# Kernel optimization log

Measured on AMD Instinct MI355X. Metric: run time of the kernel, lower is better.

Reference implementation:

```python
import jax, jax.numpy as jnp
import numpy as np

KHS = 3        # kernel_half_size
SIGMA = 1.6    # sigma / dx
DX = 1.0
C = 20.0       # accumulate() hard-codes c = 20


def _gauss_kernel():
    size = 2 * KHS + 1
    g = np.arange(size, dtype=np.float32) - (size - 1) / 2.0
    g = np.exp(-(g / SIGMA) ** 2 / 2.0) / (SIGMA * np.sqrt(2.0 * np.pi))
    k = g[:, None, None] * g[None, :, None] * g[None, None, :]
    k = k / k.sum()
    return jnp.asarray(k[None, None], dtype=jnp.float32)  # [1,1,7,7,7]


def _smooth(x, kernel):
    # depthwise (single-channel) 3d gaussian conv, 'same' padding, zero bias
    return jax.lax.conv_general_dilated(
        x, kernel, window_strides=(1, 1, 1),
        padding=[(KHS, KHS)] * 3,
        dimension_numbers=("NCDHW", "OIDHW", "NCDHW"))


def _fdiff(f, axis):
    # forward difference, replicate last difference to keep size (torchJacobian3 style)
    d = jnp.diff(f, axis=axis)
    last = jax.lax.slice_in_dim(d, d.shape[axis] - 1, d.shape[axis], axis=axis)
    return jnp.concatenate([d, last], axis=axis)


def _curl(v):
    # v: [B,3,D,H,W]; per-channel fields are [B,D,H,W]; z->axis1, y->axis2, x->axis3
    u, vv, w = v[:, 0], v[:, 1], v[:, 2]
    cu = _fdiff(w, 2) - _fdiff(vv, 1)   # dw/dy - dv/dz
    cv = _fdiff(u, 1) - _fdiff(w, 3)    # du/dz - dw/dx
    cw = _fdiff(vv, 3) - _fdiff(u, 2)   # dv/dx - du/dy
    return jnp.stack([cu, cv, cw], axis=1)


def _integrate(t, v):
    # trapezoidal transmittance-weighted integral along depth (dim 2)
    front = (1.0 - t[:, :, 0]) * v[:, :, 0]
    trap = jnp.sum((t[:, :, :-1] - t[:, :, 1:]) * (v[:, :, :-1] + v[:, :, 1:]) * 0.5, axis=2)
    return front + trap


def setup_inputs() -> dict:
    key = jax.random.key(0)
    k1, k2 = jax.random.split(key)
    d = jax.random.uniform(k1, (4, 1, 128, 128, 128), dtype=jnp.float32)
    v = jax.random.normal(k2, (4, 3, 128, 128, 128), dtype=jnp.float32)
    return {"d": d, "v": v}


def reference(d, v):
    kern = _gauss_kernel()
    ds = _smooth(d, kern)
    vort = _curl(v) / DX
    vn = jnp.sqrt(jnp.sum(vort ** 2, axis=1, keepdims=True))  # [B,1,D,H,W]
    vn = _smooth(vn, kern)
    # single default view dir 'zp' -> identity rotation
    df = jnp.flip(ds, axis=2)
    vf = jnp.flip(vn, axis=2)
    x = jnp.cumsum(df * DX, axis=2)
    t = (x * C + 1.0) * jnp.exp(-C * x)
    iv = _integrate(t, vf)              # [B,1,H,W]
    return jnp.clip(iv, 0.0, 1.0)
```

## Files before the change

kernel.cpp:

```cpp
#include <hip/hip_runtime.h>
#include <math.h>

#define NB 4
#define DD 128
#define HH 128
#define WW 128
#define VOX (DD*HH*WW)
#define NVOX (NB*VOX)

struct GaussW { float w[7]; };
struct CurlIn { float4 wc, wyn, vc, vzn, uc, uzn, uyn; float wxp, vxp; };

__device__ __forceinline__ float4 f4zero() { float4 z; z.x = z.y = z.z = z.w = 0.f; return z; }

__device__ __forceinline__ CurlIn curl4_load(const float* __restrict__ u,
                                             const float* __restrict__ vv,
                                             const float* __restrict__ w,
                                             int z, int y, int x0) {
    int xq = x0 >> 2;
    size_t s = ((size_t)z << 14) | ((size_t)y << 7) | (size_t)x0;
    int dy = (y < 127) ? 128 : -128;
    int dz = (z < 127) ? 16384 : -16384;
    int dxp = (xq < 31) ? 4 : 0;
    CurlIn ci;
    ci.wc  = *(const float4*)(w  + s);
    ci.wyn = *(const float4*)(w  + s + dy);
    ci.vc  = *(const float4*)(vv + s);
    ci.vzn = *(const float4*)(vv + s + dz);
    ci.uc  = *(const float4*)(u  + s);
    ci.uzn = *(const float4*)(u  + s + dz);
    ci.uyn = *(const float4*)(u  + s + dy);
    ci.wxp = w [s + 3 + dxp];
    ci.vxp = vv[s + 3 + dxp];
    return ci;
}

__device__ __forceinline__ float4 curl4_math(const CurlIn& ci, int z, int y, int x0) {
    float sy = (y < 127) ? 1.f : -1.f;
    float sz = (z < 127) ? 1.f : -1.f;
    float wca[4] = {ci.wc.x, ci.wc.y, ci.wc.z, ci.wc.w};
    float vca[4] = {ci.vc.x, ci.vc.y, ci.vc.z, ci.vc.w};
    float wya[4] = {ci.wyn.x, ci.wyn.y, ci.wyn.z, ci.wyn.w};
    float vza[4] = {ci.vzn.x, ci.vzn.y, ci.vzn.z, ci.vzn.w};
    float uca[4] = {ci.uc.x, ci.uc.y, ci.uc.z, ci.uc.w};
    float uza[4] = {ci.uzn.x, ci.uzn.y, ci.uzn.z, ci.uzn.w};
    float uya[4] = {ci.uyn.x, ci.uyn.y, ci.uyn.z, ci.uyn.w};
    float wsh[4] = {ci.wc.y, ci.wc.z, ci.wc.w, ci.wxp};
    float vsh[4] = {ci.vc.y, ci.vc.z, ci.vc.w, ci.vxp};

    float4 o;
    float* oa = &o.x;
#pragma unroll
    for (int j = 0; j < 4; ++j) {
        int x = x0 + j;
        float fdxw = (x < 127) ? (wsh[j] - wca[j]) : (wca[3] - wca[2]);
        float fdxv = (x < 127) ? (vsh[j] - vca[j]) : (vca[3] - vca[2]);
        float fdyw = sy * (wya[j] - wca[j]);
        float fdyu = sy * (uya[j] - uca[j]);
        float fdzv = sz * (vza[j] - vca[j]);
        float fdzu = sz * (uza[j] - uca[j]);
        float cu = fdyw - fdzv;
        float cv = fdzu - fdxw;
        float cw = fdxv - fdyu;
        oa[j] = sqrtf(cu * cu + cv * cv + cw * cw);
    }
    return o;
}

__global__ __launch_bounds__(512, 2)
void yx_curl_dual_kernel(const float* __restrict__ dIn, float* __restrict__ P,
                         const float* __restrict__ v,   float* __restrict__ Q,
                         GaussW gw) {
    __shared__ float in_t[38][128];

    const int NT = 512;
    int bb = blockIdx.x;
    bool isCurl = (bb >= 2048);
    int b  = bb & 2047;
    int yq = b & 3;
    int z  = (b >> 2) & 127;
    int n  = b >> 9;
    int y0 = yq * 32;
    size_t slice = (((size_t)n << 7) | (size_t)z) << 14;
    int tid = threadIdx.x;

    if (!isCurl) {
        float4 Ld[3];
#pragma unroll
        for (int t = 0; t < 3; ++t) {
            int j  = tid + t * NT;
            int r  = j >> 5;
            int c4 = (j & 31) << 2;
            int gy = y0 - 3 + r;
            Ld[t] = (j < 1216 && gy >= 0 && gy < 128)
                  ? *(const float4*)(dIn + slice + ((size_t)gy << 7) + c4)
                  : f4zero();
        }
#pragma unroll
        for (int t = 0; t < 3; ++t) {
            int j = tid + t * NT;
            if (j < 1216) *(float4*)&in_t[j >> 5][(j & 31) << 2] = Ld[t];
        }
    } else {
        const float* u  = v + (size_t)n * 3 * VOX;
        const float* vv = u + VOX;
        const float* w  = vv + VOX;
        CurlIn ci[3];
        bool inb[3];
#pragma unroll
        for (int t = 0; t < 3; ++t) {
            int j  = tid + t * NT;
            int r  = j >> 5;
            int c4 = (j & 31) << 2;
            int gy = y0 - 3 + r;
            inb[t] = (j < 1216 && gy >= 0 && gy < 128);
            if (inb[t]) ci[t] = curl4_load(u, vv, w, z, gy, c4);
        }
#pragma unroll
        for (int t = 0; t < 3; ++t) {
            int j  = tid + t * NT;
            if (j < 1216) {
                int r  = j >> 5;
                int c4 = (j & 31) << 2;
                int gy = y0 - 3 + r;
                float4 val = inb[t] ? curl4_math(ci[t], z, gy, c4) : f4zero();
                *(float4*)&in_t[r][c4] = val;
            }
        }
    }
    __syncthreads();

    float4 rr[2];
#pragma unroll
    for (int t = 0; t < 2; ++t) {
        int j  = tid + t * NT;
        int yo = j >> 5;
        int c4 = (j & 31) << 2;
        float4 a = f4zero();
#pragma unroll
        for (int k = 0; k < 7; ++k) {
            float wk = gw.w[k];
            float4 tv = *(const float4*)&in_t[yo + k][c4];
            a.x += wk * tv.x; a.y += wk * tv.y; a.z += wk * tv.z; a.w += wk * tv.w;
        }
        rr[t] = a;
    }
    __syncthreads();

#pragma unroll
    for (int t = 0; t < 2; ++t) {
        int j  = tid + t * NT;
        *(float4*)&in_t[j >> 5][(j & 31) << 2] = rr[t];
    }
    __syncthreads();

    float* out = isCurl ? Q : P;
#pragma unroll
    for (int t = 0; t < 2; ++t) {
        int j   = tid + t * NT;
        int yo  = j >> 5;
        int x0c = (j & 31) << 2;
        float4 q0 = (x0c > 0)   ? *(const float4*)&in_t[yo][x0c - 4] : f4zero();
        float4 q1 =               *(const float4*)&in_t[yo][x0c];
        float4 q2 = (x0c < 124) ? *(const float4*)&in_t[yo][x0c + 4] : f4zero();
        float wdw[11] = {q0.y, q0.z, q0.w,
                         q1.x, q1.y, q1.z, q1.w,
                         q2.x, q2.y, q2.z, q2.w};
        float o[4];
#pragma unroll
        for (int j2 = 0; j2 < 4; ++j2) {
            float acc = 0.f;
#pragma unroll
            for (int k = 0; k < 7; ++k) acc += gw.w[k] * wdw[j2 + k];
            o[j2] = acc;
        }
        *(float4*)(out + slice + ((size_t)(y0 + yo) << 7) + x0c) =
            make_float4(o[0], o[1], o[2], o[3]);
    }
}

__global__ __launch_bounds__(256, 4)
void render_zs4_kernel(const float* __restrict__ P, const float* __restrict__ Q,
                       float* __restrict__ out, GaussW gw) {
    __shared__ float csum[4][64];
    __shared__ float part[4][64];

    int xl = threadIdx.x & 63;
    int ch = threadIdx.x >> 6;
    int col = blockIdx.x * 64 + xl;
    int x = col & 127;
    int y = (col >> 7) & 127;
    int n = col >> 14;
    size_t volbase = ((size_t)n << 21) | ((size_t)y << 7) | (size_t)x;
    int j0 = ch * 32;

    float a[38];
#pragma unroll
    for (int t = 0; t < 38; ++t) {
        int j = j0 - 3 + t;
        a[t] = (j >= 0 && j <= 127) ? P[volbase + ((size_t)(127 - j) << 14)] : 0.f;
    }
#pragma unroll
    for (int i = 0; i < 32; ++i) {
        float s = 0.f;
#pragma unroll
        for (int k = 0; k < 7; ++k) s += gw.w[k] * a[i + k];
        a[i] = s;
    }
    float S = 0.f;
#pragma unroll
    for (int i = 0; i < 32; ++i) S += a[i];
    csum[ch][xl] = S;

    float bq[39];
#pragma unroll
    for (int t = 0; t < 39; ++t) {
        int j = j0 - 4 + t;
        bq[t] = (j >= 0 && j <= 127) ? Q[volbase + ((size_t)(127 - j) << 14)] : 0.f;
    }
    __syncthreads();

    float offset = 0.f;
    if (ch > 0) offset += csum[0][xl];
    if (ch > 1) offset += csum[1][xl];
    if (ch > 2) offset += csum[2][xl];

    float tp = 0.f, vp = 0.f, acc = 0.f, xacc = offset;
    if (ch > 0) {
        float v0 = 0.f;
#pragma unroll
        for (int k = 0; k < 7; ++k) v0 += gw.w[k] * bq[k];
        vp = v0;
        float xc = 20.f * offset;
        tp = (xc + 1.f) * __expf(-xc);
    }
#pragma unroll
    for (int i = 0; i < 32; ++i) {
        xacc += a[i];
        float vk = 0.f;
#pragma unroll
        for (int k = 0; k < 7; ++k) vk += gw.w[k] * bq[i + 1 + k];
        float xc = 20.f * xacc;
        float tk = (xc + 1.f) * __expf(-xc);
        if (ch == 0 && i == 0) acc = (1.f - tk) * vk;
        else                   acc += (tp - tk) * (vp + vk) * 0.5f;
        tp = tk; vp = vk;
    }
    part[ch][xl] = acc;
    __syncthreads();

    if (ch == 0) {
        float r = part[0][xl] + part[1][xl] + part[2][xl] + part[3][xl];
        out[col] = fminf(fmaxf(r, 0.f), 1.f);
    }
}

extern "C" void kernel_launch(void* const* d_in, const int* in_sizes, int n_in,
                              void* d_out, int out_size, void* d_ws, size_t ws_size,
                              hipStream_t stream) {
    const float* d = (const float*)d_in[0];
    const float* v = (const float*)d_in[1];
    float* out = (float*)d_out;

    GaussW gw;
    {
        double g[7], s = 0.0;
        for (int i = 0; i < 7; ++i) {
            double t = (i - 3) / 1.6;
            g[i] = exp(-t * t / 2.0);
            s += g[i];
        }
        for (int i = 0; i < 7; ++i) gw.w[i] = (float)(g[i] / s);
    }

    float* ws0 = (float*)d_ws;
    float* ws1 = ws0 + NVOX;

    yx_curl_dual_kernel<<<2 * NB * DD * 4, 512, 0, stream>>>(d, ws0, v, ws1, gw);

    render_zs4_kernel<<<(NB * HH * WW) / 64, 256, 0, stream>>>(ws0, ws1, out, gw);
}
```

Before: 191.8 us.

## Stage curl and density tiles into LDS via global_load_lds with smaller y-tiles

Replaces the register-staged global loads with direct global-to-LDS transfers (global_load_lds, 16 bytes per lane). The curl branch now stages five row-blocks (w, u, v at z and v, u at z+1) into a large shared buffer and reads y-neighbours from LDS instead of reloading them from global memory. The y-tile shrinks from 32 to 16 rows, which doubles the grid and gives one output float4 per thread. The aim is to cut VGPR pressure and redundant global traffic, at the cost of a larger halo ratio and about 71 KB of LDS per block, which may limit occupancy.

```diff
diff --git a/kernel.cpp b/kernel.cpp
--- a/kernel.cpp
+++ b/kernel.cpp
@@ -9,174 +9,176 @@
 #define NVOX (NB*VOX)
 
 struct GaussW { float w[7]; };
-struct CurlIn { float4 wc, wyn, vc, vzn, uc, uzn, uyn; float wxp, vxp; };
 
 __device__ __forceinline__ float4 f4zero() { float4 z; z.x = z.y = z.z = z.w = 0.f; return z; }
 
-__device__ __forceinline__ CurlIn curl4_load(const float* __restrict__ u,
-                                             const float* __restrict__ vv,
-                                             const float* __restrict__ w,
-                                             int z, int y, int x0) {
-    int xq = x0 >> 2;
-    size_t s = ((size_t)z << 14) | ((size_t)y << 7) | (size_t)x0;
-    int dy = (y < 127) ? 128 : -128;
-    int dz = (z < 127) ? 16384 : -16384;
-    int dxp = (xq < 31) ? 4 : 0;
-    CurlIn ci;
-    ci.wc  = *(const float4*)(w  + s);
-    ci.wyn = *(const float4*)(w  + s + dy);
-    ci.vc  = *(const float4*)(vv + s);
-    ci.vzn = *(const float4*)(vv + s + dz);
-    ci.uc  = *(const float4*)(u  + s);
-    ci.uzn = *(const float4*)(u  + s + dz);
-    ci.uyn = *(const float4*)(u  + s + dy);
-    ci.wxp = w [s + 3 + dxp];
-    ci.vxp = vv[s + 3 + dxp];
-    return ci;
-}
-
-__device__ __forceinline__ float4 curl4_math(const CurlIn& ci, int z, int y, int x0) {
-    float sy = (y < 127) ? 1.f : -1.f;
-    float sz = (z < 127) ? 1.f : -1.f;
-    float wca[4] = {ci.wc.x, ci.wc.y, ci.wc.z, ci.wc.w};
-    float vca[4] = {ci.vc.x, ci.vc.y, ci.vc.z, ci.vc.w};
-    float wya[4] = {ci.wyn.x, ci.wyn.y, ci.wyn.z, ci.wyn.w};
-    float vza[4] = {ci.vzn.x, ci.vzn.y, ci.vzn.z, ci.vzn.w};
-    float uca[4] = {ci.uc.x, ci.uc.y, ci.uc.z, ci.uc.w};
-    float uza[4] = {ci.uzn.x, ci.uzn.y, ci.uzn.z, ci.uzn.w};
-    float uya[4] = {ci.uyn.x, ci.uyn.y, ci.uyn.z, ci.uyn.w};
-    float wsh[4] = {ci.wc.y, ci.wc.z, ci.wc.w, ci.wxp};
-    float vsh[4] = {ci.vc.y, ci.vc.z, ci.vc.w, ci.vxp};
-
-    float4 o;
-    float* oa = &o.x;
-#pragma unroll
-    for (int j = 0; j < 4; ++j) {
-        int x = x0 + j;
-        float fdxw = (x < 127) ? (wsh[j] - wca[j]) : (wca[3] - wca[2]);
-        float fdxv = (x < 127) ? (vsh[j] - vca[j]) : (vca[3] - vca[2]);
-        float fdyw = sy * (wya[j] - wca[j]);
-        float fdyu = sy * (uya[j] - uca[j]);
-        float fdzv = sz * (vza[j] - vca[j]);
-        float fdzu = sz * (uza[j] - uca[j]);
-        float cu = fdyw - fdzv;
-        float cv = fdzu - fdxw;
-        float cw = fdxv - fdyu;
-        oa[j] = sqrtf(cu * cu + cv * cv + cw * cw);
-    }
-    return o;
+__device__ __forceinline__ void gll16(const float* g, float* l) {
+    __builtin_amdgcn_global_load_lds(
+        (const __attribute__((address_space(1))) unsigned int*)g,
+        (__attribute__((address_space(3))) unsigned int*)l, 16, 0, 0);
 }
 
 __global__ __launch_bounds__(512, 2)
 void yx_curl_dual_kernel(const float* __restrict__ dIn, float* __restrict__ P,
                          const float* __restrict__ v,   float* __restrict__ Q,
                          GaussW gw) {
-    __shared__ float in_t[38][128];
+    __shared__ __attribute__((aligned(16))) float stage[120 * 128];
+    __shared__ __attribute__((aligned(16))) float in_t[22][128];
 
     const int NT = 512;
     int bb = blockIdx.x;
-    bool isCurl = (bb >= 2048);
-    int b  = bb & 2047;
-    int yq = b & 3;
-    int z  = (b >> 2) & 127;
-    int n  = b >> 9;
-    int y0 = yq * 32;
+    bool isCurl = (bb >= 4096);
+    int b  = bb & 4095;
+    int yq = b & 7;
+    int z  = (b >> 3) & 127;
+    int n  = b >> 10;
+    int y0 = yq << 4;
+    size_t zoff  = (size_t)z << 14;
     size_t slice = (((size_t)n << 7) | (size_t)z) << 14;
-    int tid = threadIdx.x;
+    int tid  = threadIdx.x;
+    int wid  = tid >> 6;
+    int lane = tid & 63;
+    int lrow = lane >> 5;
+    int lcol = (lane & 31) << 2;
 
     if (!isCurl) {
-        float4 Ld[3];
-#pragma unroll
-        for (int t = 0; t < 3; ++t) {
-            int j  = tid + t * NT;
-            int r  = j >> 5;
-            int c4 = (j & 31) << 2;
-            int gy = y0 - 3 + r;
-            Ld[t] = (j < 1216 && gy >= 0 && gy < 128)
-                  ? *(const float4*)(dIn + slice + ((size_t)gy << 7) + c4)
-                  : f4zero();
-        }
-#pragma unroll
-        for (int t = 0; t < 3; ++t) {
-            int j = tid + t * NT;
-            if (j < 1216) *(float4*)&in_t[j >> 5][(j & 31) << 2] = Ld[t];
+#pragma unroll
+        for (int t = 0; t < 2; ++t) {
+            int pr = wid + (t << 3);
+            if (pr < 11) {
+                int r0 = pr << 1;
+                int gy = y0 - 3 + r0 + lrow;
+                gy = min(127, max(0, gy));
+                gll16(dIn + slice + ((size_t)gy << 7) + lcol, &in_t[r0][0]);
+            }
+        }
+        __syncthreads();
+        if (y0 == 0 || y0 == 112) {
+#pragma unroll
+            for (int t = 0; t < 2; ++t) {
+                int j = tid + t * NT;
+                if (j < 704) {
+                    int lr = j >> 5;
+                    int gy = y0 - 3 + lr;
+                    if (gy < 0 || gy > 127)
+                        *(float4*)&in_t[lr][(j & 31) << 2] = f4zero();
+                }
+            }
         }
     } else {
         const float* u  = v + (size_t)n * 3 * VOX;
         const float* vv = u + VOX;
         const float* w  = vv + VOX;
-        CurlIn ci[3];
-        bool inb[3];
-#pragma unroll
-        for (int t = 0; t < 3; ++t) {
-            int j  = tid + t * NT;
-            int r  = j >> 5;
-            int c4 = (j & 31) << 2;
-            int gy = y0 - 3 + r;
-            inb[t] = (j < 1216 && gy >= 0 && gy < 128);
-            if (inb[t]) ci[t] = curl4_load(u, vv, w, z, gy, c4);
-        }
-#pragma unroll
-        for (int t = 0; t < 3; ++t) {
-            int j  = tid + t * NT;
-            if (j < 1216) {
-                int r  = j >> 5;
+        int dzo = (z < 127) ? 16384 : -16384;
+        const float* b0 = w  + zoff;
+        const float* b1 = u  + zoff;
+        const float* b2 = vv + zoff;
+        const float* b3 = vv + zoff + dzo;
+        const float* b4 = u  + zoff + dzo;
+#pragma unroll
+        for (int t = 0; t < 8; ++t) {
+            int pr = wid + (t << 3);
+            if (pr < 60) {
+                int buf = pr / 12;
+                int r0  = (pr - buf * 12) << 1;
+                int gy  = y0 - 3 + r0 + lrow;
+                gy = min(127, max(0, gy));
+                const float* bp = (buf == 0) ? b0 : (buf == 1) ? b1
+                                : (buf == 2) ? b2 : (buf == 3) ? b3 : b4;
+                gll16(bp + ((size_t)gy << 7) + lcol,
+                      stage + (((buf * 24) + r0) << 7));
+            }
+        }
+        __syncthreads();
+
+        float sz = (z < 127) ? 1.f : -1.f;
+        const float* sW  = stage;
+        const float* sU  = stage + 24 * 128;
+        const float* sVc = stage + 48 * 128;
+        const float* sVz = stage + 72 * 128;
+        const float* sUz = stage + 96 * 128;
+#pragma unroll
+        for (int t = 0; t < 2; ++t) {
+            int j = tid + t * NT;
+            if (j < 704) {
+                int lr = j >> 5;
                 int c4 = (j & 31) << 2;
-                int gy = y0 - 3 + r;
-                float4 val = inb[t] ? curl4_math(ci[t], z, gy, c4) : f4zero();
-                *(float4*)&in_t[r][c4] = val;
-            }
-        }
-    }
-    __syncthreads();
-
-    float4 rr[2];
-#pragma unroll
-    for (int t = 0; t < 2; ++t) {
-        int j  = tid + t * NT;
-        int yo = j >> 5;
-        int c4 = (j & 31) << 2;
-        float4 a = f4zero();
-#pragma unroll
-        for (int k = 0; k < 7; ++k) {
-            float wk = gw.w[k];
-            float4 tv = *(const float4*)&in_t[yo + k][c4];
-            a.x += wk * tv.x; a.y += wk * tv.y; a.z += wk * tv.z; a.w += wk * tv.w;
-        }
-        rr[t] = a;
-    }
-    __syncthreads();
-
-#pragma unroll
-    for (int t = 0; t < 2; ++t) {
-        int j  = tid + t * NT;
-        *(float4*)&in_t[j >> 5][(j & 31) << 2] = rr[t];
-    }
+                int gy = y0 - 3 + lr;
+                float4 val;
+                if (gy >= 0 && gy <= 127) {
+                    int   ry = (gy < 127) ? lr + 1 : lr - 1;
+                    float sy = (gy < 127) ? 1.f : -1.f;
+                    int ro = lr << 7, ryo = ry << 7;
+                    float4 wc  = *(const float4*)(sW  + ro  + c4);
+                    float4 wy  = *(const float4*)(sW  + ryo + c4);
+                    float4 uc  = *(const float4*)(sU  + ro  + c4);
+                    float4 uy  = *(const float4*)(sU  + ryo + c4);
+                    float4 vc  = *(const float4*)(sVc + ro  + c4);
+                    float4 vzn = *(const float4*)(sVz + ro  + c4);
+                    float4 uzn = *(const float4*)(sUz + ro  + c4);
+                    float wxp = sW [ro + c4 + 4];
+                    float vxp = sVc[ro + c4 + 4];
+                    float wca[4] = {wc.x, wc.y, wc.z, wc.w};
+                    float vca[4] = {vc.x, vc.y, vc.z, vc.w};
+                    float wya[4] = {wy.x, wy.y, wy.z, wy.w};
+                    float vza[4] = {vzn.x, vzn.y, vzn.z, vzn.w};
+                    float uca[4] = {uc.x, uc.y, uc.z, uc.w};
+                    float uza[4] = {uzn.x, uzn.y, uzn.z, uzn.w};
+                    float uya[4] = {uy.x, uy.y, uy.z, uy.w};
+                    float wsh[4] = {wc.y, wc.z, wc.w, wxp};
+                    float vsh[4] = {vc.y, vc.z, vc.w, vxp};
+                    float* oa = &val.x;
+#pragma unroll
+                    for (int j2 = 0; j2 < 4; ++j2) {
+                        int x = c4 + j2;
+                        float fdxw = (x < 127) ? (wsh[j2] - wca[j2]) : (wca[3] - wca[2]);
+                        float fdxv = (x < 127) ? (vsh[j2] - vca[j2]) : (vca[3] - vca[2]);
+                        float fdyw = sy * (wya[j2] - wca[j2]);
+                        float fdyu = sy * (uya[j2] - uca[j2]);
+                        float fdzv = sz * (vza[j2] - vca[j2]);
+                        float fdzu = sz * (uza[j2] - uca[j2]);
+                        float cu = fdyw - fdzv;
+                        float cv = fdzu - fdxw;
+                        float cw = fdxv - fdyu;
+                        oa[j2] = sqrtf(cu * cu + cv * cv + cw * cw);
+                    }
+                } else val = f4zero();
+                *(float4*)&in_t[lr][c4] = val;
+            }
+        }
+    }
+    __syncthreads();
+
+    int yo = tid >> 5;
+    int c4 = (tid & 31) << 2;
+    float4 a = f4zero();
+#pragma unroll
+    for (int k = 0; k < 7; ++k) {
+        float wk = gw.w[k];
+        float4 tv = *(const float4*)&in_t[yo + k][c4];
+        a.x += wk * tv.x; a.y += wk * tv.y; a.z += wk * tv.z; a.w += wk * tv.w;
+    }
+    __syncthreads();
+    *(float4*)&in_t[yo][c4] = a;
     __syncthreads();
 
     float* out = isCurl ? Q : P;
-#pragma unroll
-    for (int t = 0; t < 2; ++t) {
-        int j   = tid + t * NT;
-        int yo  = j >> 5;
-        int x0c = (j & 31) << 2;
-        float4 q0 = (x0c > 0)   ? *(const float4*)&in_t[yo][x0c - 4] : f4zero();
-        float4 q1 =               *(const float4*)&in_t[yo][x0c];
-        float4 q2 = (x0c < 124) ? *(const float4*)&in_t[yo][x0c + 4] : f4zero();
-        float wdw[11] = {q0.y, q0.z, q0.w,
-                         q1.x, q1.y, q1.z, q1.w,
-                         q2.x, q2.y, q2.z, q2.w};
-        float o[4];
-#pragma unroll
-        for (int j2 = 0; j2 < 4; ++j2) {
-            float acc = 0.f;
-#pragma unroll
-            for (int k = 0; k < 7; ++k) acc += gw.w[k] * wdw[j2 + k];
-            o[j2] = acc;
-        }
-        *(float4*)(out + slice + ((size_t)(y0 + yo) << 7) + x0c) =
-            make_float4(o[0], o[1], o[2], o[3]);
-    }
+    float4 q0 = (c4 > 0)   ? *(const float4*)&in_t[yo][c4 - 4] : f4zero();
+    float4 q1 =              *(const float4*)&in_t[yo][c4];
+    float4 q2 = (c4 < 124) ? *(const float4*)&in_t[yo][c4 + 4] : f4zero();
+    float wdw[11] = {q0.y, q0.z, q0.w,
+                     q1.x, q1.y, q1.z, q1.w,
+                     q2.x, q2.y, q2.z, q2.w};
+    float o[4];
+#pragma unroll
+    for (int j2 = 0; j2 < 4; ++j2) {
+        float acc = 0.f;
+#pragma unroll
+        for (int k = 0; k < 7; ++k) acc += gw.w[k] * wdw[j2 + k];
+        o[j2] = acc;
+    }
+    *(float4*)(out + slice + ((size_t)(y0 + yo) << 7) + c4) =
+        make_float4(o[0], o[1], o[2], o[3]);
 }
 
 __global__ __launch_bounds__(256, 4)
@@ -276,7 +278,7 @@
     float* ws0 = (float*)d_ws;
     float* ws1 = ws0 + NVOX;
 
-    yx_curl_dual_kernel<<<2 * NB * DD * 4, 512, 0, stream>>>(d, ws0, v, ws1, gw);
+    yx_curl_dual_kernel<<<2 * NB * DD * 8, 512, 0, stream>>>(d, ws0, v, ws1, gw);
 
     render_zs4_kernel<<<(NB * HH * WW) / 64, 256, 0, stream>>>(ws0, ws1, out, gw);
 }
```

Result: slower. 196.5 us (+2.5%).
